# Performance work log

Measured on AMD Instinct MI355X. Metric: run time of the kernel, lower is better.

The kernel has to match this reference:

```python
import jax, jax.numpy as jnp
import numpy as np

N, F, K = 256, 32, 8
B = 65536


def setup_inputs() -> dict:
    key = jax.random.key(0)
    k1, k2, k3, k4 = jax.random.split(key, 4)
    x = jax.random.normal(k1, (B, N), dtype=jnp.float32)
    w_lin = jax.random.normal(k2, (N,), dtype=jnp.float32)
    b_lin = jax.random.normal(k3, (1,), dtype=jnp.float32)
    v = jax.random.normal(k4, (N, F, K), dtype=jnp.float32)
    # feature -> field mapping, matching feature2fielddict = {i: i % F}
    field_idx = jnp.arange(N, dtype=jnp.int32) % F
    return {"x": x, "w_lin": w_lin, "b_lin": b_lin, "v": v, "field_idx": field_idx}


def reference(x, w_lin, b_lin, v, field_idx):
    # linear part: nn.Linear(n, 1)
    linear_part = x @ w_lin[:, None] + b_lin  # [B, 1]
    # A[i, j] = v[i, field[j]]  -> [n, n, k]
    A = v[:, field_idx, :]
    # Wmat[i, j] = <v[i, field[j]], v[j, field[i]]>
    Wmat = jnp.einsum('ijk,jik->ij', A, A)  # [n, n]
    # only strict upper triangle (i < j) contributes
    Wu = jnp.triu(Wmat, k=1)
    # sum_{i<j} Wmat[i,j] * x[:,i] * x[:,j]
    interaction = jnp.einsum('bi,ij,bj->b', x, Wu, x)[:, None]  # [B, 1]
    return linear_part + interaction
```

## Files before the change

kernel.cpp:

```cpp
#include <hip/hip_runtime.h>
#include <hip/hip_bf16.h>


#define FK 256

typedef __attribute__((ext_vector_type(8))) short bf16x8;
typedef __attribute__((ext_vector_type(4))) float f32x4v;

__device__ __forceinline__ unsigned short f2bf(float x) {
    return __builtin_bit_cast(unsigned short, __float2bfloat16(x));
}
__device__ __forceinline__ float bf2f(unsigned short h) {
    return __builtin_bit_cast(float, (unsigned int)h << 16);
}

template<int CTRL>
__device__ __forceinline__ float dppadd(float v) {
    int t = __builtin_amdgcn_update_dpp(0, __builtin_bit_cast(int, v),
                                        CTRL, 0xf, 0xf, true);
    return v + __builtin_bit_cast(float, t);
}

__global__ __launch_bounds__(64) void k_build_m(
    const float* __restrict__ v, const int* __restrict__ fidx,
    uint2* __restrict__ mpack2)
{
    int t = blockIdx.x * 64 + threadIdx.x;
    int h  = t & 1;
    int l  = (t >> 1) & 63;
    int ct = (t >> 7) & 15;
    int s  = t >> 11;
    int c  = ct * 16 + (l & 15);
    int k0 = s * 32 + ((l >> 4) & 3) * 8 + h * 4;
    int fc = fidx[c];
    unsigned short hh[4];
#pragma unroll
    for (int i = 0; i < 4; ++i) {
        int k = k0 + i;
        float acc = 0.f;
        if (k != c) {
            int fk = fidx[k];
            const float* va = v + k * FK + fc * 8;
            const float* vb = v + c * FK + fk * 8;
#pragma unroll
            for (int j = 0; j < 8; ++j) acc += va[j] * vb[j];
            acc *= 0.5f;
        }
        hh[i] = f2bf(acc);
    }
    uint2 o;
    o.x = (unsigned int)hh[0] | ((unsigned int)hh[1] << 16);
    o.y = (unsigned int)hh[2] | ((unsigned int)hh[3] << 16);
    mpack2[t] = o;
}


struct SmemT {
    unsigned short xs[2][4096];
    float part[2][8][16];
};

__device__ __forceinline__ void stage_write(unsigned short* buf, float4 val,
                                            int row, int chunk) {
    unsigned long long h0 = f2bf(val.x), h1 = f2bf(val.y),
                       h2 = f2bf(val.z), h3 = f2bf(val.w);
    unsigned long long pk = h0 | (h1 << 16) | (h2 << 32) | (h3 << 48);
    int byteoff = row * 512 + ((chunk * 8) ^ ((row & 7) << 4));
    *(unsigned long long*)((char*)buf + byteoff) = pk;
}

__global__ __launch_bounds__(512, 4) void k_main(
    const float* __restrict__ x, const float* __restrict__ w_lin,
    const float* __restrict__ b_lin, const uint4* __restrict__ mpack,
    float* __restrict__ out)
{
    __shared__ SmemT sm;

    const int tid = threadIdx.x;
    const int w   = tid >> 6;
    const int l   = tid & 63;
    const int l15 = l & 15;
    const int lg  = l >> 4;

    bf16x8 Brg[8][2];
#pragma unroll
    for (int s = 0; s < 8; ++s)
#pragma unroll
        for (int ct = 0; ct < 2; ++ct)
            Brg[s][ct] = __builtin_bit_cast(bf16x8,
                mpack[(s * 16 + w * 2 + ct) * 64 + l]);

    const float w0 = w_lin[(w * 2 + 0) * 16 + l15];
    const float w1 = w_lin[(w * 2 + 1) * 16 + l15];
    const float bv = b_lin[0];

    const long rowbase = (long)blockIdx.x * 128;
    const float* xg = x + rowbase * 256;

    const int srow = w * 2 + (l >> 5);
    const int sc0  = l & 31;
    const int sc1  = sc0 + 32;

    float4 pa = *(const float4*)(xg + srow * 256 + sc0 * 4);
    float4 pb = *(const float4*)(xg + srow * 256 + sc1 * 4);
    stage_write(sm.xs[0], pa, srow, sc0);
    stage_write(sm.xs[0], pb, srow, sc1);
    pa = *(const float4*)(xg + (16 + srow) * 256 + sc0 * 4);
    pb = *(const float4*)(xg + (16 + srow) * 256 + sc1 * 4);
    __syncthreads();

    for (int t = 0; t < 8; ++t) {
        const char* xsb = (const char*)sm.xs[t & 1];

        f32x4v acc0 = {w0, w0, w0, w0};
        f32x4v acc1 = {w1, w1, w1, w1};
#pragma unroll
        for (int s = 0; s < 8; ++s) {
            int aoff = l15 * 512 + ((s * 64 + lg * 16) ^ ((l15 & 7) << 4));
            bf16x8 af = *(const bf16x8*)(xsb + aoff);
            acc0 = __builtin_amdgcn_mfma_f32_16x16x32_bf16(af, Brg[s][0], acc0, 0, 0, 0);
            acc1 = __builtin_amdgcn_mfma_f32_16x16x32_bf16(af, Brg[s][1], acc1, 0, 0, 0);
        }

#pragma unroll
        for (int r = 0; r < 4; ++r) {
            int row = lg * 4 + r;
            int sw  = (row & 7) << 4;
            int c0  = (w * 2 + 0) * 16 + l15;
            int c1  = (w * 2 + 1) * 16 + l15;
            unsigned short h0 = *(const unsigned short*)(xsb + row * 512 + ((c0 * 2) ^ sw));
            unsigned short h1 = *(const unsigned short*)(xsb + row * 512 + ((c1 * 2) ^ sw));
            float pp = bf2f(h0) * acc0[r] + bf2f(h1) * acc1[r];
            pp = dppadd<0x121>(pp); pp = dppadd<0x122>(pp);
            pp = dppadd<0x124>(pp); pp = dppadd<0x128>(pp);
            if (l15 == 0) sm.part[t & 1][w][row] = pp;
        }

        if (t < 7) {
            unsigned short* nb = sm.xs[(t + 1) & 1];
            stage_write(nb, pa, srow, sc0);
            stage_write(nb, pb, srow, sc1);
        }
        if (t < 6) {
            pa = *(const float4*)(xg + ((t + 2) * 16 + srow) * 256 + sc0 * 4);
            pb = *(const float4*)(xg + ((t + 2) * 16 + srow) * 256 + sc1 * 4);
        }
        __syncthreads();

        if (tid < 16) {
            const float (*pt)[16] = sm.part[t & 1];
            float y = pt[0][tid] + pt[1][tid] + pt[2][tid] + pt[3][tid] +
                      pt[4][tid] + pt[5][tid] + pt[6][tid] + pt[7][tid];
            out[rowbase + t * 16 + tid] = y + bv;
        }
    }
}

extern "C" void kernel_launch(void* const* d_in, const int* in_sizes, int n_in,
                              void* d_out, int out_size, void* d_ws, size_t ws_size,
                              hipStream_t stream) {
    const float* x     = (const float*)d_in[0];
    const float* w_lin = (const float*)d_in[1];
    const float* b_lin = (const float*)d_in[2];
    const float* v     = (const float*)d_in[3];
    const int*   fidx  = (const int*)d_in[4];
    float* out = (float*)d_out;
    void* mpack = d_ws;

    k_build_m<<<256, 64, 0, stream>>>(v, fidx, (uint2*)mpack);
    k_main<<<512, 512, 0, stream>>>(x, w_lin, b_lin, (const uint4*)mpack, out);
}
```

Measured before the change: 23.69 us.

## Deepen x prefetch to two tiles, use lgkm-only barriers, widen build kernel

The main kernel now keeps two register prefetch buffers, loading x tiles two steps ahead instead of one, and issues the first x loads before the matrix register loads. It also fully unrolls the tile loop. Block barriers now wait only on LDS counters rather than on outstanding global loads, so prefetches stay in flight across a barrier. The build kernel caches field indices in shared memory and uses twice as many threads, each computing two entries. The cost is more live registers under the 512x4 launch bound, and the custom barrier depends on the compiler inserting vmcnt waits before prefetched values are used.

Result: slower. 38.18 us (+61.2%).

```diff
diff --git a/kernel.cpp b/kernel.cpp
--- a/kernel.cpp
+++ b/kernel.cpp
@@ -21,25 +21,36 @@
     return v + __builtin_bit_cast(float, t);
 }
 
-__global__ __launch_bounds__(64) void k_build_m(
+__device__ __forceinline__ void block_sync_novm() {
+    asm volatile("s_waitcnt lgkmcnt(0)\n\ts_barrier" ::: "memory");
+}
+
+__global__ __launch_bounds__(128) void k_build_m(
     const float* __restrict__ v, const int* __restrict__ fidx,
-    uint2* __restrict__ mpack2)
+    unsigned int* __restrict__ mp)
 {
-    int t = blockIdx.x * 64 + threadIdx.x;
-    int h  = t & 1;
-    int l  = (t >> 1) & 63;
-    int ct = (t >> 7) & 15;
-    int s  = t >> 11;
+    __shared__ int fsh[256];
+    int tid = threadIdx.x;
+    fsh[tid] = fidx[tid];
+    fsh[tid + 128] = fidx[tid + 128];
+    __syncthreads();
+
+    int u = blockIdx.x * 128 + tid;
+    int f  = u >> 2;
+    int l  = f & 63;
+    int ct = (f >> 6) & 15;
+    int s  = f >> 10;
     int c  = ct * 16 + (l & 15);
-    int k0 = s * 32 + ((l >> 4) & 3) * 8 + h * 4;
-    int fc = fidx[c];
-    unsigned short hh[4];
+    int i80 = (u & 3) * 2;
+    int k0 = s * 32 + ((l >> 4) & 3) * 8 + i80;
+    int fc = fsh[c];
+    unsigned short hh[2];
 #pragma unroll
-    for (int i = 0; i < 4; ++i) {
+    for (int i = 0; i < 2; ++i) {
         int k = k0 + i;
         float acc = 0.f;
         if (k != c) {
-            int fk = fidx[k];
+            int fk = fsh[k];
             const float* va = v + k * FK + fc * 8;
             const float* vb = v + c * FK + fk * 8;
 #pragma unroll
@@ -48,10 +59,7 @@
         }
         hh[i] = f2bf(acc);
     }
-    uint2 o;
-    o.x = (unsigned int)hh[0] | ((unsigned int)hh[1] << 16);
-    o.y = (unsigned int)hh[2] | ((unsigned int)hh[3] << 16);
-    mpack2[t] = o;
+    mp[u] = (unsigned int)hh[0] | ((unsigned int)hh[1] << 16);
 }
 
 
@@ -82,6 +90,16 @@
     const int l15 = l & 15;
     const int lg  = l >> 4;
 
+    const long rowbase = (long)blockIdx.x * 128;
+    const float* xg = x + rowbase * 256;
+
+    const int srow = w * 2 + (l >> 5);
+    const int sc0  = l & 31;
+    const int sc1  = sc0 + 32;
+
+    float4 a0 = *(const float4*)(xg + srow * 256 + sc0 * 4);
+    float4 b0 = *(const float4*)(xg + srow * 256 + sc1 * 4);
+
     bf16x8 Brg[8][2];
 #pragma unroll
     for (int s = 0; s < 8; ++s)
@@ -90,25 +108,20 @@
             Brg[s][ct] = __builtin_bit_cast(bf16x8,
                 mpack[(s * 16 + w * 2 + ct) * 64 + l]);
 
+    float4 Pa1 = *(const float4*)(xg + (16 + srow) * 256 + sc0 * 4);
+    float4 Pb1 = *(const float4*)(xg + (16 + srow) * 256 + sc1 * 4);
+    float4 Pa0 = *(const float4*)(xg + (32 + srow) * 256 + sc0 * 4);
+    float4 Pb0 = *(const float4*)(xg + (32 + srow) * 256 + sc1 * 4);
+
     const float w0 = w_lin[(w * 2 + 0) * 16 + l15];
     const float w1 = w_lin[(w * 2 + 1) * 16 + l15];
     const float bv = b_lin[0];
 
-    const long rowbase = (long)blockIdx.x * 128;
-    const float* xg = x + rowbase * 256;
+    stage_write(sm.xs[0], a0, srow, sc0);
+    stage_write(sm.xs[0], b0, srow, sc1);
+    block_sync_novm();
 
-    const int srow = w * 2 + (l >> 5);
-    const int sc0  = l & 31;
-    const int sc1  = sc0 + 32;
-
-    float4 pa = *(const float4*)(xg + srow * 256 + sc0 * 4);
-    float4 pb = *(const float4*)(xg + srow * 256 + sc1 * 4);
-    stage_write(sm.xs[0], pa, srow, sc0);
-    stage_write(sm.xs[0], pb, srow, sc1);
-    pa = *(const float4*)(xg + (16 + srow) * 256 + sc0 * 4);
-    pb = *(const float4*)(xg + (16 + srow) * 256 + sc1 * 4);
-    __syncthreads();
-
+#pragma unroll
     for (int t = 0; t < 8; ++t) {
         const char* xsb = (const char*)sm.xs[t & 1];
 
@@ -138,14 +151,23 @@
 
         if (t < 7) {
             unsigned short* nb = sm.xs[(t + 1) & 1];
-            stage_write(nb, pa, srow, sc0);
-            stage_write(nb, pb, srow, sc1);
+            if (((t + 1) & 1) == 0) {
+                stage_write(nb, Pa0, srow, sc0);
+                stage_write(nb, Pb0, srow, sc1);
+                if (t < 5) {
+                    Pa0 = *(const float4*)(xg + ((t + 3) * 16 + srow) * 256 + sc0 * 4);
+                    Pb0 = *(const float4*)(xg + ((t + 3) * 16 + srow) * 256 + sc1 * 4);
+                }
+            } else {
+                stage_write(nb, Pa1, srow, sc0);
+                stage_write(nb, Pb1, srow, sc1);
+                if (t < 5) {
+                    Pa1 = *(const float4*)(xg + ((t + 3) * 16 + srow) * 256 + sc0 * 4);
+                    Pb1 = *(const float4*)(xg + ((t + 3) * 16 + srow) * 256 + sc1 * 4);
+                }
+            }
         }
-        if (t < 6) {
-            pa = *(const float4*)(xg + ((t + 2) * 16 + srow) * 256 + sc0 * 4);
-            pb = *(const float4*)(xg + ((t + 2) * 16 + srow) * 256 + sc1 * 4);
-        }
-        __syncthreads();
+        block_sync_novm();
 
         if (tid < 16) {
             const float (*pt)[16] = sm.part[t & 1];
@@ -167,6 +189,6 @@
     float* out = (float*)d_out;
     void* mpack = d_ws;
 
-    k_build_m<<<256, 64, 0, stream>>>(v, fidx, (uint2*)mpack);
+    k_build_m<<<256, 128, 0, stream>>>(v, fidx, (unsigned int*)mpack);
     k_main<<<512, 512, 0, stream>>>(x, w_lin, b_lin, (const uint4*)mpack, out);
 }
```
